# Kernel tuning notes

Hardware: AMD Instinct MI355X
Metric: run time of the kernel (lower is better)

The kernel has to match this reference:

```python
import jax, jax.numpy as jnp
import numpy as np

T, B, H, L = 200, 32, 1024, 2
DROPOUT = 0.32
KEEP = 1.0 - DROPOUT
FORGET_GATE_BIAS = 1.0


def setup_inputs() -> dict:
    key = jax.random.key(0)
    ks = jax.random.split(key, 8)
    scale = 1.0 / np.sqrt(H)  # torch LSTM default init: U(-1/sqrt(H), 1/sqrt(H))
    x = jax.random.normal(ks[0], (T, B, H), jnp.float32)
    W_ih = jax.random.uniform(ks[1], (L, 4 * H, H), jnp.float32, -scale, scale)
    W_hh = jax.random.uniform(ks[2], (L, 4 * H, H), jnp.float32, -scale, scale)
    b_ih = jax.random.uniform(ks[3], (L, 4 * H), jnp.float32, -scale, scale)
    b_hh = jax.random.uniform(ks[4], (L, 4 * H), jnp.float32, -scale, scale)
    # forget-gate bias init as in LstmDrop.__init__ (gate order i,f,g,o)
    b_ih = b_ih.at[:, H:2 * H].set(FORGET_GATE_BIAS)
    b_hh = b_hh.at[:, H:2 * H].set(0.0)
    h0 = jnp.zeros((L, B, H), jnp.float32)
    c0 = jnp.zeros((L, B, H), jnp.float32)
    # inverted dropout masks: inter-layer (torch LSTM dropout, applied to all but last layer)
    # and the trailing inplace Dropout on the output sequence
    mask_inter = (jax.random.bernoulli(ks[5], KEEP, (L - 1, T, B, H)) / KEEP).astype(jnp.float32)
    mask_out = (jax.random.bernoulli(ks[6], KEEP, (T, B, H)) / KEEP).astype(jnp.float32)
    return {"x": x, "h0": h0, "c0": c0, "W_ih": W_ih, "W_hh": W_hh,
            "b_ih": b_ih, "b_hh": b_hh, "mask_inter": mask_inter, "mask_out": mask_out}


def _lstm_layer(xs, h, c, Wih, Whh, b):
    # xs: [T,B,in]; Wih/Whh: [4H,in]/[4H,H]; b: [4H] (b_ih + b_hh fused)
    def step(carry, x_t):
        h, c = carry
        gates = x_t @ Wih.T + h @ Whh.T + b  # [B,4H]
        i, f, g, o = jnp.split(gates, 4, axis=-1)
        c = jax.nn.sigmoid(f) * c + jax.nn.sigmoid(i) * jnp.tanh(g)
        h = jax.nn.sigmoid(o) * jnp.tanh(c)
        return (h, c), h
    (hT, cT), ys = jax.lax.scan(step, (h, c), xs)
    return ys, hT, cT


def reference(x, h0, c0, W_ih, W_hh, b_ih, b_hh, mask_inter, mask_out):
    y = x
    h_last, c_last = [], []
    for l in range(L):
        y, hT, cT = _lstm_layer(y, h0[l], c0[l], W_ih[l], W_hh[l], b_ih[l] + b_hh[l])
        h_last.append(hT)
        c_last.append(cT)
        if l < L - 1:  # torch LSTM applies dropout between layers only
            y = y * mask_inter[l]
    y = y * mask_out  # the inplace Dropout on the output sequence
    return y, jnp.stack(h_last), jnp.stack(c_last)
```

## Files before the change

### kernel.cpp

```cpp
#include <hip/hip_runtime.h>

#define T_STEPS 200
#define BATCH   32
#define HID     1024
#define NWG     256
#define NTHR    512

typedef _Float16 half8 __attribute__((ext_vector_type(8)));
typedef float    f32x4 __attribute__((ext_vector_type(4)));

struct Bar {
    unsigned cnt[2][8 * 32];
    unsigned gcnt[2 * 32];
    unsigned gen[8 * 32];
};

__device__ __forceinline__ half8 ld_coh16(const _Float16* p) {
    union { unsigned long long u[2]; half8 h; } r;
    const unsigned long long* q = (const unsigned long long*)p;
    r.u[0] = __hip_atomic_load(q,     __ATOMIC_RELAXED, __HIP_MEMORY_SCOPE_AGENT);
    r.u[1] = __hip_atomic_load(q + 1, __ATOMIC_RELAXED, __HIP_MEMORY_SCOPE_AGENT);
    return r.h;
}
__device__ __forceinline__ void st_coh16(_Float16* p, half8 v) {
    union { half8 h; unsigned long long u[2]; } r; r.h = v;
    unsigned long long* q = (unsigned long long*)p;
    __hip_atomic_store(q,     r.u[0], __ATOMIC_RELAXED, __HIP_MEMORY_SCOPE_AGENT);
    __hip_atomic_store(q + 1, r.u[1], __ATOMIC_RELAXED, __HIP_MEMORY_SCOPE_AGENT);
}

__device__ __forceinline__ half8 cvt8(const float* p) {
    f32x4 lo = *(const f32x4*)p;
    f32x4 hi = *(const f32x4*)(p + 4);
    half8 a;
    a[0] = (_Float16)lo[0]; a[1] = (_Float16)lo[1];
    a[2] = (_Float16)lo[2]; a[3] = (_Float16)lo[3];
    a[4] = (_Float16)hi[0]; a[5] = (_Float16)hi[1];
    a[6] = (_Float16)hi[2]; a[7] = (_Float16)hi[3];
    return a;
}

__global__ void init_k(const float* __restrict__ h0,
                       _Float16* __restrict__ h0b, _Float16* __restrict__ h1b,
                       Bar* __restrict__ bar) {
    int i = blockIdx.x * blockDim.x + threadIdx.x;
    if (i < BATCH * HID) {
        h0b[i] = (_Float16)h0[i];
        h1b[i] = (_Float16)h0[BATCH * HID + i];
    }
    if (blockIdx.x == 0) {
        if (threadIdx.x < 8) {
            bar->cnt[0][threadIdx.x * 32] = 0;
            bar->cnt[1][threadIdx.x * 32] = 0;
            bar->gen[threadIdx.x * 32]    = 0;
        }
        if (threadIdx.x < 2) bar->gcnt[threadIdx.x * 32] = 0;
    }
}

__global__ __launch_bounds__(NTHR, 2) void lstm_main(
    const float* __restrict__ x, const float* __restrict__ c0,
    const float* __restrict__ Wih, const float* __restrict__ Whh,
    const float* __restrict__ bih, const float* __restrict__ bhh,
    const float* __restrict__ mi, const float* __restrict__ mo,
    float* __restrict__ out,
    _Float16* __restrict__ y0m, _Float16* __restrict__ h0b,
    _Float16* __restrict__ h1b, Bar* __restrict__ bar)
{
    __shared__ _Float16 W_s[32 * 2048];
    __shared__ float scr[8][2][16][17];
    __shared__ float c_s[BATCH][8];
    __shared__ alignas(16) _Float16 st_h[BATCH][8];
    __shared__ alignas(16) _Float16 st_y[BATCH][8];
    __shared__ unsigned rel_flag;

    const int bid   = blockIdx.x;
    const int layer = bid >> 7;
    const int wgl   = bid & 127;
    const int tid   = threadIdx.x;

    if (tid == 0) rel_flag = 0;

    const float* WihL = Wih + (size_t)layer * 4 * HID * HID;
    const float* WhhL = Whh + (size_t)layer * 4 * HID * HID;
    for (int idx = tid; idx < 32 * 2048; idx += NTHR) {
        int r = idx >> 11, k = idx & 2047;
        int grow = (r >> 3) * HID + wgl * 8 + (r & 7);
        float v = (k < HID) ? WihL[(size_t)grow * HID + k]
                            : WhhL[(size_t)grow * HID + (k - HID)];
        W_s[idx ^ ((r & 7) << 3)] = (_Float16)v;
    }

    float bias0 = 0.f, bias1 = 0.f, bias2 = 0.f, bias3 = 0.f;
    int b_ = 0, col_ = 0, gcol = 0;
    if (tid < 256) {
        b_ = tid >> 3; col_ = tid & 7; gcol = wgl * 8 + col_;
        bias0 = bih[layer * 4096 + gcol]           + bhh[layer * 4096 + gcol];
        bias1 = bih[layer * 4096 + HID + gcol]     + bhh[layer * 4096 + HID + gcol];
        bias2 = bih[layer * 4096 + 2 * HID + gcol] + bhh[layer * 4096 + 2 * HID + gcol];
        bias3 = bih[layer * 4096 + 3 * HID + gcol] + bhh[layer * 4096 + 3 * HID + gcol];
        c_s[b_][col_] = c0[((size_t)layer * BATCH + b_) * HID + gcol];
    }
    __syncthreads();

    const int lane = tid & 63, wid = tid >> 6;
    const int m  = wid & 1;
    const int kq = wid >> 1;
    const int row = lane & 15, bb = m * 16 + row, ko = (lane >> 4) * 8;
    const int grp = bid & 7;

    for (int tk = 0; tk <= T_STEPS; ++tk) {
        const bool active = (layer == 0) ? (tk < T_STEPS) : (tk >= 1);
        if (active) {
            const int t = (layer == 0) ? tk : tk - 1;
            const _Float16* hrd = (layer == 0) ? (h0b + (tk & 1) * (BATCH * HID))
                                               : (h1b + (((tk + 1) & 1)) * (BATCH * HID));
            f32x4 acc0 = {0.f, 0.f, 0.f, 0.f}, acc1 = {0.f, 0.f, 0.f, 0.f};

            half8 aF[16];
            if (kq < 2) {
                if (layer == 0) {
                    const float* xp = x + ((size_t)t * BATCH + bb) * HID + kq * 512 + ko;
                    #pragma unroll
                    for (int kk = 0; kk < 16; ++kk) aF[kk] = cvt8(xp + kk * 32);
                } else {
                    const _Float16* yp = y0m + ((size_t)t * BATCH + bb) * HID + kq * 512 + ko;
                    #pragma unroll
                    for (int kk = 0; kk < 16; ++kk) aF[kk] = ld_coh16(yp + kk * 32);
                }
            } else {
                const _Float16* hp = hrd + bb * HID + (kq - 2) * 512 + ko;
                #pragma unroll
                for (int kk = 0; kk < 16; ++kk) aF[kk] = ld_coh16(hp + kk * 32);
            }

            #pragma unroll
            for (int kk = 0; kk < 16; ++kk) {
                const int k  = kq * 512 + kk * 32 + ko;
                const int r1 = 16 + row;
                const half8 b0 = *(const half8*)&W_s[(row * 2048 + k) ^ ((row & 7) << 3)];
                const half8 b1 = *(const half8*)&W_s[(r1 * 2048 + k) ^ ((r1 & 7) << 3)];
                acc0 = __builtin_amdgcn_mfma_f32_16x16x32_f16(aF[kk], b0, acc0, 0, 0, 0);
                acc1 = __builtin_amdgcn_mfma_f32_16x16x32_f16(aF[kk], b1, acc1, 0, 0, 0);
            }
            #pragma unroll
            for (int j = 0; j < 4; ++j) {
                scr[wid][0][(lane >> 4) * 4 + j][row] = acc0[j];
                scr[wid][1][(lane >> 4) * 4 + j][row] = acc1[j];
            }
            __syncthreads();

            if (tid < 256) {
                const int m2 = b_ >> 4, rD = b_ & 15;
                float v0 = 0.f, v1 = 0.f, v2 = 0.f, v3 = 0.f;
                #pragma unroll
                for (int q = 0; q < 4; ++q) {
                    v0 += scr[q * 2 + m2][0][rD][col_];
                    v1 += scr[q * 2 + m2][0][rD][8 + col_];
                    v2 += scr[q * 2 + m2][1][rD][col_];
                    v3 += scr[q * 2 + m2][1][rD][8 + col_];
                }
                const float ig = 1.f / (1.f + __expf(-(v0 + bias0)));
                const float fg = 1.f / (1.f + __expf(-(v1 + bias1)));
                const float gg = tanhf(v2 + bias2);
                const float og = 1.f / (1.f + __expf(-(v3 + bias3)));
                const float cc = fg * c_s[b_][col_] + ig * gg;
                const float hh = og * tanhf(cc);
                c_s[b_][col_] = cc;

                st_h[b_][col_] = (_Float16)hh;

                const size_t oidx = ((size_t)t * BATCH + b_) * HID + gcol;
                if (layer == 0) {
                    st_y[b_][col_] = (_Float16)(hh * mi[oidx]);
                } else {
                    out[oidx] = hh * mo[oidx];
                }
                if (t == T_STEPS - 1) {
                    const size_t base = (size_t)T_STEPS * BATCH * HID;
                    out[base + ((size_t)layer * BATCH + b_) * HID + gcol] = hh;
                    out[base + (size_t)2 * BATCH * HID + ((size_t)layer * BATCH + b_) * HID + gcol] = cc;
                }
            }
            __syncthreads();

            if (tid < BATCH) {
                _Float16* hwr = (layer == 0) ? (h0b + (((tk + 1) & 1)) * (BATCH * HID))
                                             : (h1b + ((tk & 1)) * (BATCH * HID));
                st_coh16(&hwr[tid * HID + wgl * 8], *(const half8*)st_h[tid]);
                if (layer == 0)
                    st_coh16(&y0m[((size_t)t * BATCH + tid) * HID + wgl * 8],
                             *(const half8*)st_y[tid]);
            }
        }

        if (tk == T_STEPS) break;

        const unsigned tgt = (unsigned)(tk + 1);
        const int p = tk & 1;

        if (wid == 0) {
            int pubi = 0;
            if (lane == 0) {
                asm volatile("s_waitcnt vmcnt(0)" ::: "memory");
                unsigned old = __hip_atomic_fetch_add(&bar->cnt[p][grp * 32], 1u,
                                   __ATOMIC_RELAXED, __HIP_MEMORY_SCOPE_AGENT);
                if (old == 31u) {
                    unsigned o2 = __hip_atomic_fetch_add(&bar->gcnt[p * 32], 1u,
                                       __ATOMIC_RELAXED, __HIP_MEMORY_SCOPE_AGENT);
                    pubi = (o2 == 7u) ? 1 : 0;
                }
            }
            pubi = __shfl(pubi, 0);
            if (pubi) {
                if (lane < 8)
                    __hip_atomic_store(&bar->gen[lane * 32], tgt,
                                       __ATOMIC_RELAXED, __HIP_MEMORY_SCOPE_AGENT);
                else if (lane < 16)
                    __hip_atomic_store(&bar->cnt[p][(lane - 8) * 32], 0u,
                                       __ATOMIC_RELAXED, __HIP_MEMORY_SCOPE_AGENT);
                else if (lane == 16)
                    __hip_atomic_store(&bar->gcnt[p * 32], 0u,
                                       __ATOMIC_RELAXED, __HIP_MEMORY_SCOPE_AGENT);
            }
            if (lane == 0) {
                if (!pubi) {
                    float j0 = 0.f, j1 = 0.f;
                    while (__hip_atomic_load(&bar->gen[grp * 32], __ATOMIC_RELAXED,
                                             __HIP_MEMORY_SCOPE_AGENT) < tgt) {
                        asm volatile("v_fma_f32 %0,%0,%0,%0\n"
                                     "v_fma_f32 %1,%1,%1,%1\n"
                                     "v_fma_f32 %0,%0,%0,%0\n"
                                     "v_fma_f32 %1,%1,%1,%1"
                                     : "+v"(j0), "+v"(j1));
                    }
                }
                *(volatile unsigned*)&rel_flag = tgt;
            }
        } else {
            float j0 = 0.f, j1 = 0.f, j2 = 0.f, j3 = 0.f;
            while (*(volatile unsigned*)&rel_flag < tgt) {
                asm volatile("v_fma_f32 %0,%0,%0,%0\n"
                             "v_fma_f32 %1,%1,%1,%1\n"
                             "v_fma_f32 %2,%2,%2,%2\n"
                             "v_fma_f32 %3,%3,%3,%3\n"
                             "v_fma_f32 %0,%0,%0,%0\n"
                             "v_fma_f32 %1,%1,%1,%1\n"
                             "v_fma_f32 %2,%2,%2,%2\n"
                             "v_fma_f32 %3,%3,%3,%3"
                             : "+v"(j0), "+v"(j1), "+v"(j2), "+v"(j3));
            }
        }
        asm volatile("" ::: "memory");
        __syncthreads();
    }
}

extern "C" void kernel_launch(void* const* d_in, const int* in_sizes, int n_in,
                              void* d_out, int out_size, void* d_ws, size_t ws_size,
                              hipStream_t stream) {
    const float* x   = (const float*)d_in[0];
    const float* h0  = (const float*)d_in[1];
    const float* c0  = (const float*)d_in[2];
    const float* Wih = (const float*)d_in[3];
    const float* Whh = (const float*)d_in[4];
    const float* bih = (const float*)d_in[5];
    const float* bhh = (const float*)d_in[6];
    const float* mi  = (const float*)d_in[7];
    const float* mo  = (const float*)d_in[8];
    float* out = (float*)d_out;

    char* w = (char*)d_ws;
    _Float16* y0m = (_Float16*)w;
    _Float16* h0b = (_Float16*)(w + 13107200);
    _Float16* h1b = (_Float16*)(w + 13107200 + 131072);
    Bar*      bar = (Bar*)(w + 13107200 + 262144);

    hipLaunchKernelGGL(init_k, dim3(128), dim3(256), 0, stream, h0, h0b, h1b, bar);

    void* args[] = {(void*)&x, (void*)&c0, (void*)&Wih, (void*)&Whh,
                    (void*)&bih, (void*)&bhh, (void*)&mi, (void*)&mo,
                    (void*)&out, (void*)&y0m, (void*)&h0b, (void*)&h1b, (void*)&bar};
    hipLaunchCooperativeKernel((void*)lstm_main, dim3(NWG), dim3(NTHR),
                               args, 0, stream);
}
```

Before: 2.177 ms.

## Prefetch next-step x and dropout masks during barrier wait, offload output stores

Layer-0 waves now load and convert the next timestep's x slice and inter-layer mask into registers while spinning on the grid barrier, so these global loads leave the serial critical path. Layer-1 output dropout is moved to the otherwise idle upper 256 threads, which prefetch the mask during the wait and write the output after staging h in shared memory. This adds register pressure (aF kept live across iterations) and extra shared-memory traffic. Wave 0 also prefetches before its spin, which may delay the barrier release slightly.

```diff
diff --git a/kernel.cpp b/kernel.cpp
--- a/kernel.cpp
+++ b/kernel.cpp
@@ -72,6 +72,7 @@
     __shared__ float c_s[BATCH][8];
     __shared__ alignas(16) _Float16 st_h[BATCH][8];
     __shared__ alignas(16) _Float16 st_y[BATCH][8];
+    __shared__ float st_o[BATCH][8];
     __shared__ unsigned rel_flag;
 
     const int bid   = blockIdx.x;
@@ -101,6 +102,9 @@
         bias3 = bih[layer * 4096 + 3 * HID + gcol] + bhh[layer * 4096 + 3 * HID + gcol];
         c_s[b_][col_] = c0[((size_t)layer * BATCH + b_) * HID + gcol];
     }
+    const int ot = tid - 256;
+    const int b2 = (ot >= 0) ? (ot >> 3) : 0, c2 = (ot >= 0) ? (ot & 7) : 0;
+    const int gcol2 = wgl * 8 + c2;
     __syncthreads();
 
     const int lane = tid & 63, wid = tid >> 6;
@@ -109,39 +113,50 @@
     const int row = lane & 15, bb = m * 16 + row, ko = (lane >> 4) * 8;
     const int grp = bid & 7;
 
+    half8 aF[16];
+    float mi_reg = 0.f, mo_reg = 0.f;
+    if (layer == 0) {
+        if (kq < 2) {
+            const float* xp = x + (size_t)bb * HID + kq * 512 + ko;
+            #pragma unroll
+            for (int kk = 0; kk < 16; ++kk) aF[kk] = cvt8(xp + kk * 32);
+        }
+        if (tid < 256) mi_reg = mi[(size_t)b_ * HID + gcol];
+    }
+
     for (int tk = 0; tk <= T_STEPS; ++tk) {
         const bool active = (layer == 0) ? (tk < T_STEPS) : (tk >= 1);
         if (active) {
             const int t = (layer == 0) ? tk : tk - 1;
-            const _Float16* hrd = (layer == 0) ? (h0b + (tk & 1) * (BATCH * HID))
-                                               : (h1b + (((tk + 1) & 1)) * (BATCH * HID));
-            f32x4 acc0 = {0.f, 0.f, 0.f, 0.f}, acc1 = {0.f, 0.f, 0.f, 0.f};
-
-            half8 aF[16];
-            if (kq < 2) {
-                if (layer == 0) {
-                    const float* xp = x + ((size_t)t * BATCH + bb) * HID + kq * 512 + ko;
+            if (layer == 0) {
+                if (kq >= 2) {
+                    const _Float16* hp = h0b + (tk & 1) * (BATCH * HID)
+                                       + bb * HID + (kq - 2) * 512 + ko;
                     #pragma unroll
-                    for (int kk = 0; kk < 16; ++kk) aF[kk] = cvt8(xp + kk * 32);
-                } else {
+                    for (int kk = 0; kk < 16; ++kk) aF[kk] = ld_coh16(hp + kk * 32);
+                }
+            } else {
+                if (kq < 2) {
                     const _Float16* yp = y0m + ((size_t)t * BATCH + bb) * HID + kq * 512 + ko;
                     #pragma unroll
                     for (int kk = 0; kk < 16; ++kk) aF[kk] = ld_coh16(yp + kk * 32);
-                }
-            } else {
-                const _Float16* hp = hrd + bb * HID + (kq - 2) * 512 + ko;
-                #pragma unroll
-                for (int kk = 0; kk < 16; ++kk) aF[kk] = ld_coh16(hp + kk * 32);
-            }
-
+                } else {
+                    const _Float16* hp = h1b + (((tk + 1) & 1)) * (BATCH * HID)
+                                       + bb * HID + (kq - 2) * 512 + ko;
+                    #pragma unroll
+                    for (int kk = 0; kk < 16; ++kk) aF[kk] = ld_coh16(hp + kk * 32);
+                }
+            }
+
+            f32x4 acc0 = {0.f, 0.f, 0.f, 0.f}, acc1 = {0.f, 0.f, 0.f, 0.f};
             #pragma unroll
             for (int kk = 0; kk < 16; ++kk) {
                 const int k  = kq * 512 + kk * 32 + ko;
                 const int r1 = 16 + row;
-                const half8 b0 = *(const half8*)&W_s[(row * 2048 + k) ^ ((row & 7) << 3)];
-                const half8 b1 = *(const half8*)&W_s[(r1 * 2048 + k) ^ ((r1 & 7) << 3)];
-                acc0 = __builtin_amdgcn_mfma_f32_16x16x32_f16(aF[kk], b0, acc0, 0, 0, 0);
-                acc1 = __builtin_amdgcn_mfma_f32_16x16x32_f16(aF[kk], b1, acc1, 0, 0, 0);
+                const half8 bB0 = *(const half8*)&W_s[(row * 2048 + k) ^ ((row & 7) << 3)];
+                const half8 bB1 = *(const half8*)&W_s[(r1 * 2048 + k) ^ ((r1 & 7) << 3)];
+                acc0 = __builtin_amdgcn_mfma_f32_16x16x32_f16(aF[kk], bB0, acc0, 0, 0, 0);
+                acc1 = __builtin_amdgcn_mfma_f32_16x16x32_f16(aF[kk], bB1, acc1, 0, 0, 0);
             }
             #pragma unroll
             for (int j = 0; j < 4; ++j) {
@@ -169,12 +184,10 @@
                 c_s[b_][col_] = cc;
 
                 st_h[b_][col_] = (_Float16)hh;
-
-                const size_t oidx = ((size_t)t * BATCH + b_) * HID + gcol;
                 if (layer == 0) {
-                    st_y[b_][col_] = (_Float16)(hh * mi[oidx]);
+                    st_y[b_][col_] = (_Float16)(hh * mi_reg);
                 } else {
-                    out[oidx] = hh * mo[oidx];
+                    st_o[b_][col_] = hh;
                 }
                 if (t == T_STEPS - 1) {
                     const size_t base = (size_t)T_STEPS * BATCH * HID;
@@ -191,6 +204,9 @@
                 if (layer == 0)
                     st_coh16(&y0m[((size_t)t * BATCH + tid) * HID + wgl * 8],
                              *(const half8*)st_y[tid]);
+            }
+            if (layer == 1 && ot >= 0) {
+                out[((size_t)t * BATCH + b2) * HID + gcol2] = st_o[b2][c2] * mo_reg;
             }
         }
 
@@ -223,6 +239,13 @@
                     __hip_atomic_store(&bar->gcnt[p * 32], 0u,
                                        __ATOMIC_RELAXED, __HIP_MEMORY_SCOPE_AGENT);
             }
+            if (layer == 0 && kq < 2 && tk + 1 < T_STEPS) {
+                const float* xp = x + ((size_t)(tk + 1) * BATCH + bb) * HID + kq * 512 + ko;
+                #pragma unroll
+                for (int kk = 0; kk < 16; ++kk) aF[kk] = cvt8(xp + kk * 32);
+            }
+            if (layer == 0 && tid < 256 && tk + 1 < T_STEPS)
+                mi_reg = mi[((size_t)(tk + 1) * BATCH + b_) * HID + gcol];
             if (lane == 0) {
                 if (!pubi) {
                     float j0 = 0.f, j1 = 0.f;
@@ -238,6 +261,18 @@
                 *(volatile unsigned*)&rel_flag = tgt;
             }
         } else {
+            if (layer == 0) {
+                if (kq < 2 && tk + 1 < T_STEPS) {
+                    const float* xp = x + ((size_t)(tk + 1) * BATCH + bb) * HID + kq * 512 + ko;
+                    #pragma unroll
+                    for (int kk = 0; kk < 16; ++kk) aF[kk] = cvt8(xp + kk * 32);
+                }
+                if (tid < 256 && tk + 1 < T_STEPS)
+                    mi_reg = mi[((size_t)(tk + 1) * BATCH + b_) * HID + gcol];
+            } else {
+                if (ot >= 0 && tk < T_STEPS)
+                    mo_reg = mo[((size_t)tk * BATCH + b2) * HID + gcol2];
+            }
             float j0 = 0.f, j1 = 0.f, j2 = 0.f, j3 = 0.f;
             while (*(volatile unsigned*)&rel_flag < tgt) {
                 asm volatile("v_fma_f32 %0,%0,%0,%0\n"
```

Measured after the change: 2.148 ms. No clear change (-1.3%).
